# Kernel optimization log

Hardware: AMD Instinct MI355X
Metric: run time of the kernel (lower is better)

## Reference

```python
import jax, jax.numpy as jnp
import numpy as np

N_NODES = 20000
N_INPUT = 64
K_MAX = 12
BITS = 64
N_OUT = 10
BATCH = 64
T = 128


def setup_inputs() -> dict:
    key = jax.random.key(0)
    ks = jax.random.split(key, 8)
    x = jax.random.randint(ks[0], (BATCH, T, BITS), 0, 2, dtype=jnp.int32)
    w_in = jax.random.randint(ks[1], (BITS, N_INPUT), 0, 2, dtype=jnp.int32)
    adj_list = jax.random.randint(ks[2], (N_NODES, K_MAX), 0, N_NODES, dtype=jnp.int32)
    adj_mask = jax.random.randint(ks[3], (N_NODES, K_MAX), 0, 2, dtype=jnp.int32)
    lut = jax.random.randint(ks[4], (N_NODES, 2 ** K_MAX), 0, 2, dtype=jnp.int32)
    init_states = jax.random.randint(ks[5], (1, N_NODES), 0, 2, dtype=jnp.int32)
    W_out = jax.random.normal(ks[6], (N_OUT, N_NODES - N_INPUT), dtype=jnp.float32) * 0.02
    b_out = jnp.zeros((N_OUT,), dtype=jnp.float32)
    return {"x": x, "w_in": w_in, "adj_list": adj_list, "adj_mask": adj_mask,
            "lut": lut, "init_states": init_states, "W_out": W_out, "b_out": b_out}


def reference(x, w_in, adj_list, adj_mask, lut, init_states, W_out, b_out):
    B, T_, bits = x.shape
    N, k = adj_list.shape
    I = w_in.shape[1]
    # powers_of_2, big-endian order as in make_minimal_powers_of_two (flip)
    powers = (2 ** jnp.arange(k - 1, -1, -1)).astype(jnp.int32)  # [k]
    no_neigh = ~(adj_mask.astype(bool).any(axis=1))              # [N] nodes w/o neighbours keep state
    node_ids = jnp.arange(N)
    states0 = jnp.broadcast_to(init_states, (B, N)).astype(jnp.int32)

    def step(states, x_t):
        # inject input: bipartite mapping of input bits onto first I nodes (OR-combine)
        u = ((x_t @ w_in) > 0).astype(jnp.int32)                 # [B, I]
        states = states.at[:, :I].set(u)
        # gather incoming neighbour states per node (irregular gather)
        neigh = jnp.take(states, adj_list, axis=1)               # [B, N, k]
        neigh = neigh * adj_mask[None, :, :]
        # bit-pack into LUT index
        idx = (neigh * powers[None, None, :]).sum(axis=-1)       # [B, N], < 2^k
        new = lut[node_ids[None, :], idx]                        # [B, N] LUT lookup
        new = jnp.where(no_neigh[None, :], states, new)
        return new, None

    states, _ = jax.lax.scan(step, states0, jnp.swapaxes(x, 0, 1))
    # readout on reservoir (non-input) nodes at final timestep
    feats = states[:, I:].astype(jnp.float32)                    # [B, N-I]
    out = jax.nn.sigmoid(feats @ W_out.T + b_out)                # [B, n_outputs]
    return out
```

## Files before the change

### kernel.cpp

```cpp
#include <hip/hip_runtime.h>
#include <cstdint>
#include <cstddef>


#define N_NODES   20000
#define N_INPUT   64
#define K_MAX     12
#define T_STEPS   128
#define N_BATCH   64
#define N_OUT     10
#define N_FEAT    (N_NODES - N_INPUT)
#define DUMMY_NODE 20000
#define ST_WORDS  20004

#define NBLK 256
#define NTHR 1024
#define NPB  78
#define NPB_PAD 80
#define LEAF_CNT 64
#define GO_CNT  8
#define BAR_STRIDE 32
#define ROOT_IDX 64

typedef unsigned long long u64;

__global__ __launch_bounds__(256) void pack_x_kernel(const int* __restrict__ x,
                                                     u64* __restrict__ xp) {
  const int t = blockIdx.x;
  const int wave = threadIdx.x >> 6, lane = threadIdx.x & 63;
  for (int b = wave; b < N_BATCH; b += 4) {
    int v = x[((size_t)b * T_STEPS + t) * 64 + lane];
    u64 bal = __ballot(v != 0);
    if (lane == 0) xp[(size_t)t * N_BATCH + b] = bal;
  }
}

__global__ __launch_bounds__(256) void init_kernel(const int* __restrict__ inis,
                                                   const int* __restrict__ w_in,
                                                   u64* __restrict__ buf0,
                                                   u64* __restrict__ buf1,
                                                   u64* __restrict__ wcol,
                                                   unsigned* __restrict__ bar) {
  if (blockIdx.x < 79) {
    int n = blockIdx.x * 256 + threadIdx.x;
    if (n >= N_INPUT && n < ST_WORDS) {
      u64 w = (n < N_NODES && inis[n] != 0) ? ~0ull : 0ull;
      buf0[n] = w;
      buf1[n] = w;
    }
  } else {
    const int wave = threadIdx.x >> 6, lane = threadIdx.x & 63;
    for (int i = wave; i < 64; i += 4) {
      int wv = w_in[(size_t)lane * 64 + i];
      u64 wc = __ballot(wv != 0);
      if (lane == 0) wcol[i] = wc;
    }
    if (threadIdx.x < ROOT_IDX + 1 + GO_CNT)
      bar[threadIdx.x * BAR_STRIDE] = 0u;
  }
}

__global__ __launch_bounds__(64) void u_pre_kernel(const u64* __restrict__ xp,
                                                   const u64* __restrict__ wcol,
                                                   u64* __restrict__ u_all) {
  const int t = blockIdx.x, lane = threadIdx.x;
  u64 xw = xp[(size_t)t * N_BATCH + lane];
  for (int i = 0; i < 64; i++) {
    u64 ub = __ballot((xw & wcol[i]) != 0);
    if (lane == 0) u_all[(size_t)t * 64 + i] = ub;
  }
}

__device__ __forceinline__ u64 bit_transpose64(u64 w, int lane) {
  const u64 LO0 = 0x00000000FFFFFFFFull, LO1 = 0x0000FFFF0000FFFFull,
            LO2 = 0x00FF00FF00FF00FFull, LO3 = 0x0F0F0F0F0F0F0F0Full,
            LO4 = 0x3333333333333333ull, LO5 = 0x5555555555555555ull;
#define XP_STAGE(d, LO)                                                  \
  {                                                                      \
    u64 p = (u64)__shfl_xor((long long)w, (d), 64);                      \
    if (lane & (d)) w = ((p >> (d)) & (LO)) | (w & ~(LO));               \
    else            w = (w & (LO)) | ((p << (d)) & ~(LO));               \
  }
  XP_STAGE(32, LO0) XP_STAGE(16, LO1) XP_STAGE(8, LO2)
  XP_STAGE(4,  LO3) XP_STAGE(2,  LO4) XP_STAGE(1, LO5)
#undef XP_STAGE
  return w;
}

__global__ __launch_bounds__(NTHR) void reservoir_kernel(
    const int* __restrict__ lut, const int* __restrict__ adj,
    const int* __restrict__ mask, const u64* __restrict__ u_all,
    u64* __restrict__ buf0, u64* __restrict__ buf1,
    unsigned* __restrict__ bar) {
  __shared__ u64 lut_lds[NPB_PAD * 64];
  __shared__ int adj_lds[NPB_PAD * K_MAX];
  __shared__ unsigned char hn_lds[NPB_PAD];

  const int bi = blockIdx.x;
  const int tid = threadIdx.x;
  const int wave = tid >> 6, lane = tid & 63;
  const int base = N_INPUT + bi * NPB;
  const int nloc = min(NPB, N_NODES - base);

  if (tid < NPB_PAD) {
    int i = tid, h = 0;
    if (i < nloc) {
      for (int j = 0; j < K_MAX; j++) {
        int m = mask[(size_t)(base + i) * K_MAX + j];
        int a = adj[(size_t)(base + i) * K_MAX + j];
        adj_lds[i * K_MAX + (K_MAX - 1 - j)] = m ? a : DUMMY_NODE;
        h |= m;
      }
    } else {
      for (int j = 0; j < K_MAX; j++) adj_lds[i * K_MAX + j] = DUMMY_NODE;
    }
    hn_lds[i] = (unsigned char)(h ? 1 : 0);
  }

  const int nwords = nloc * 64;
  const int* lp = lut + (size_t)base * 4096;
  for (int w0 = wave * 8; w0 < nwords; w0 += 128) {
    int v[8];
#pragma unroll
    for (int q = 0; q < 8; q++) {
      int widx = w0 + q;
      v[q] = (widx < nwords) ? lp[(size_t)widx * 64 + lane] : 0;
    }
#pragma unroll
    for (int q = 0; q < 8; q++) {
      int widx = w0 + q;
      u64 bal = __ballot(v[q] != 0);
      if (lane == 0 && widx < nwords) lut_lds[widx] = bal;
    }
  }
  __syncthreads();

  const int l0 = wave * 5;
  const int cnt = min(5, nloc - l0);
  const bool do_store = (lane < cnt) && hn_lds[l0 + lane];

  for (int t = 0; t < T_STEPS; t++) {
    u64* cur = (t & 1) ? buf1 : buf0;
    u64* nxt = (t & 1) ? buf0 : buf1;
    const u64* ubase = u_all + (size_t)t * 64;

    u64 w = 0;
    if (lane < 60) {
      int a = adj_lds[l0 * K_MAX + lane];
      const u64* p = (a < N_INPUT) ? (ubase + a) : (cur + a);
      w = __hip_atomic_load(p, __ATOMIC_RELAXED, __HIP_MEMORY_SCOPE_AGENT);
    }
    w = bit_transpose64(w, lane);

    u64 keep = 0;
#pragma unroll
    for (int i = 0; i < 5; i++) {
      if (i < cnt) {
        unsigned idx = (unsigned)(w >> (12 * i)) & 0xFFFu;
        u64 g = lut_lds[(l0 + i) * 64 + (idx >> 6)];
        u64 res = __ballot((g >> (idx & 63)) & 1ull);
        if (lane == i) keep = res;
      }
    }
    if (do_store)
      __hip_atomic_store(&nxt[base + l0 + lane], keep,
                         __ATOMIC_RELAXED, __HIP_MEMORY_SCOPE_AGENT);

    if (t != T_STEPS - 1) {
      __syncthreads();
      __builtin_amdgcn_fence(__ATOMIC_RELEASE, "workgroup");
      if (wave == 0) {
        unsigned leafold = 0;
        if (lane == 0)
          leafold = __hip_atomic_fetch_add(&bar[(bi & (LEAF_CNT - 1)) * BAR_STRIDE],
                                           1u, __ATOMIC_RELAXED, __HIP_MEMORY_SCOPE_AGENT);
        leafold = (unsigned)__shfl((int)leafold, 0);
        if (leafold == (unsigned)t * (NBLK / LEAF_CNT) + (NBLK / LEAF_CNT - 1)) {
          unsigned rootold = 0;
          if (lane == 0)
            rootold = __hip_atomic_fetch_add(&bar[ROOT_IDX * BAR_STRIDE], 1u,
                                             __ATOMIC_RELAXED, __HIP_MEMORY_SCOPE_AGENT);
          rootold = (unsigned)__shfl((int)rootold, 0);
          if (rootold == (unsigned)t * LEAF_CNT + (LEAF_CNT - 1) && lane < GO_CNT)
            __hip_atomic_store(&bar[(ROOT_IDX + 1 + lane) * BAR_STRIDE],
                               (unsigned)(t + 1),
                               __ATOMIC_RELAXED, __HIP_MEMORY_SCOPE_AGENT);
        }
        unsigned* gp = &bar[(ROOT_IDX + 1 + (bi & (GO_CNT - 1))) * BAR_STRIDE];
        while (__hip_atomic_load(gp, __ATOMIC_RELAXED, __HIP_MEMORY_SCOPE_AGENT)
               < (unsigned)(t + 1))
          __builtin_amdgcn_s_sleep(1);
      }
      __builtin_amdgcn_fence(__ATOMIC_ACQUIRE, "workgroup");
      __syncthreads();
    }
  }
}

__global__ __launch_bounds__(256) void readout_kernel(const u64* __restrict__ st,
                                                      const float* __restrict__ Wout,
                                                      const float* __restrict__ bout,
                                                      float* __restrict__ out) {
  const int b = blockIdx.x / N_OUT;
  const int o = blockIdx.x % N_OUT;
  float acc = 0.f;
  for (int n = threadIdx.x; n < N_FEAT; n += 256) {
    u64 s = st[N_INPUT + n];
    float w = Wout[(size_t)o * N_FEAT + n];
    acc += ((s >> b) & 1ull) ? w : 0.f;
  }
  for (int off = 32; off > 0; off >>= 1) acc += __shfl_down(acc, off);
  __shared__ float red[4];
  const int wave = threadIdx.x >> 6, lane = threadIdx.x & 63;
  if (lane == 0) red[wave] = acc;
  __syncthreads();
  if (threadIdx.x == 0) {
    float tot = red[0] + red[1] + red[2] + red[3] + bout[o];
    out[(size_t)b * N_OUT + o] = 1.f / (1.f + __expf(-tot));
  }
}

extern "C" void kernel_launch(void* const* d_in, const int* in_sizes, int n_in,
                              void* d_out, int out_size, void* d_ws, size_t ws_size,
                              hipStream_t stream) {
  const int* x    = (const int*)d_in[0];
  const int* w_in = (const int*)d_in[1];
  const int* adj  = (const int*)d_in[2];
  const int* mask = (const int*)d_in[3];
  const int* lut  = (const int*)d_in[4];
  const int* inis = (const int*)d_in[5];
  const float* Wout = (const float*)d_in[6];
  const float* bout = (const float*)d_in[7];
  float* out = (float*)d_out;

  char* ws = (char*)d_ws;
  size_t off = 0;
  auto alloc = [&](size_t bytes) -> void* {
    void* p = ws + off;
    off += (bytes + 255) & ~(size_t)255;
    return p;
  };
  u64* buf0 = (u64*)alloc((size_t)ST_WORDS * 8);
  u64* buf1 = (u64*)alloc((size_t)ST_WORDS * 8);
  u64* xp   = (u64*)alloc((size_t)T_STEPS * N_BATCH * 8);
  u64* wcol = (u64*)alloc(64 * 8);
  u64* u_all = (u64*)alloc((size_t)T_STEPS * 64 * 8);
  unsigned* bar = (unsigned*)alloc((size_t)(ROOT_IDX + 1 + GO_CNT) * BAR_STRIDE * 4);
  (void)ws_size; (void)in_sizes; (void)n_in; (void)out_size;

  hipLaunchKernelGGL(pack_x_kernel, dim3(T_STEPS), dim3(256), 0, stream, x, xp);
  hipLaunchKernelGGL(init_kernel, dim3(80), dim3(256), 0, stream,
                     inis, w_in, buf0, buf1, wcol, bar);
  hipLaunchKernelGGL(u_pre_kernel, dim3(T_STEPS), dim3(64), 0, stream,
                     xp, wcol, u_all);

  void* args[] = {(void*)&lut, (void*)&adj, (void*)&mask, (void*)&u_all,
                  (void*)&buf0, (void*)&buf1, (void*)&bar};
  hipLaunchCooperativeKernel((const void*)reservoir_kernel,
                             dim3(NBLK), dim3(NTHR), args, 0, stream);

  hipLaunchKernelGGL(readout_kernel, dim3(N_BATCH * N_OUT), dim3(256), 0, stream,
                     buf0, Wout, bout, out);
}
```

Baseline: 1.061 ms.

## Replace per-step grid barrier with tagged ring-buffer dataflow sync

Each node state is split into two 64-bit words that carry 32 state bits and the timestep as a tag. Consumers spin on their neighbour loads until the tags match, which replaces the per-step global tree barrier. An 8-deep ring of state buffers lets blocks run ahead, so a flat arrival/go barrier is needed only every 6 steps to keep writers from overwriting slots still being read. This trades barrier latency for twice the gather loads, possible repeated polling of stale words, and a bounded spin guard that could silently return stale data.

```diff
diff --git a/kernel.cpp b/kernel.cpp
--- a/kernel.cpp
+++ b/kernel.cpp
@@ -17,12 +17,15 @@
 #define NTHR 1024
 #define NPB  78
 #define NPB_PAD 80
-#define LEAF_CNT 64
-#define GO_CNT  8
-#define BAR_STRIDE 32
-#define ROOT_IDX 64
+#define R_BUF 8
+#define M_BAR 6
+#define GO_CNT 8
+#define AS     32
 
 typedef unsigned long long u64;
+
+#define A_LOAD(p)    __hip_atomic_load((p), __ATOMIC_RELAXED, __HIP_MEMORY_SCOPE_AGENT)
+#define A_STORE(p,v) __hip_atomic_store((p), (v), __ATOMIC_RELAXED, __HIP_MEMORY_SCOPE_AGENT)
 
 __global__ __launch_bounds__(256) void pack_x_kernel(const int* __restrict__ x,
                                                      u64* __restrict__ xp) {
@@ -37,26 +40,34 @@
 
 __global__ __launch_bounds__(256) void init_kernel(const int* __restrict__ inis,
                                                    const int* __restrict__ w_in,
-                                                   u64* __restrict__ buf0,
-                                                   u64* __restrict__ buf1,
+                                                   const u64* __restrict__ xp,
+                                                   u64* __restrict__ Ar,
+                                                   u64* __restrict__ Br,
                                                    u64* __restrict__ wcol,
-                                                   unsigned* __restrict__ bar) {
+                                                   unsigned* __restrict__ arr,
+                                                   unsigned* __restrict__ go) {
   if (blockIdx.x < 79) {
     int n = blockIdx.x * 256 + threadIdx.x;
     if (n >= N_INPUT && n < ST_WORDS) {
       u64 w = (n < N_NODES && inis[n] != 0) ? ~0ull : 0ull;
-      buf0[n] = w;
-      buf1[n] = w;
+      Ar[n] = (w & 0xFFFFFFFFull) << 32;
+      Br[n] = (w >> 32) << 32;
     }
   } else {
     const int wave = threadIdx.x >> 6, lane = threadIdx.x & 63;
+    u64 xw = xp[lane];
     for (int i = wave; i < 64; i += 4) {
       int wv = w_in[(size_t)lane * 64 + i];
       u64 wc = __ballot(wv != 0);
       if (lane == 0) wcol[i] = wc;
-    }
-    if (threadIdx.x < ROOT_IDX + 1 + GO_CNT)
-      bar[threadIdx.x * BAR_STRIDE] = 0u;
+      u64 ub = __ballot((xw & wc) != 0);
+      if (lane == 0) {
+        Ar[i] = (ub & 0xFFFFFFFFull) << 32;
+        Br[i] = (ub >> 32) << 32;
+      }
+    }
+    arr[threadIdx.x * AS] = 0u;
+    if (threadIdx.x < GO_CNT) go[threadIdx.x * AS] = 0u;
   }
 }
 
@@ -89,12 +100,14 @@
 
 __global__ __launch_bounds__(NTHR) void reservoir_kernel(
     const int* __restrict__ lut, const int* __restrict__ adj,
-    const int* __restrict__ mask, const u64* __restrict__ u_all,
-    u64* __restrict__ buf0, u64* __restrict__ buf1,
-    unsigned* __restrict__ bar) {
+    const int* __restrict__ mask, const int* __restrict__ inis,
+    const u64* __restrict__ u_all, u64* __restrict__ Aring,
+    u64* __restrict__ Bring, unsigned* __restrict__ arr,
+    unsigned* __restrict__ go) {
   __shared__ u64 lut_lds[NPB_PAD * 64];
   __shared__ int adj_lds[NPB_PAD * K_MAX];
   __shared__ unsigned char hn_lds[NPB_PAD];
+  __shared__ volatile unsigned lds_scan[4];
 
   const int bi = blockIdx.x;
   const int tid = threadIdx.x;
@@ -116,6 +129,7 @@
     }
     hn_lds[i] = (unsigned char)(h ? 1 : 0);
   }
+  if (tid < 4) lds_scan[tid] = 0u;
 
   const int nwords = nloc * 64;
   const int* lp = lut + (size_t)base * 4096;
@@ -136,68 +150,104 @@
   __syncthreads();
 
   const int l0 = wave * 5;
-  const int cnt = min(5, nloc - l0);
-  const bool do_store = (lane < cnt) && hn_lds[l0 + lane];
-
-  for (int t = 0; t < T_STEPS; t++) {
-    u64* cur = (t & 1) ? buf1 : buf0;
-    u64* nxt = (t & 1) ? buf0 : buf1;
-    const u64* ubase = u_all + (size_t)t * 64;
-
-    u64 w = 0;
-    if (lane < 60) {
-      int a = adj_lds[l0 * K_MAX + lane];
-      const u64* p = (a < N_INPUT) ? (ubase + a) : (cur + a);
-      w = __hip_atomic_load(p, __ATOMIC_RELAXED, __HIP_MEMORY_SCOPE_AGENT);
-    }
-    w = bit_transpose64(w, lane);
-
-    u64 keep = 0;
+  const int cnt5 = min(5, nloc - l0);
+  const int a_reg = (lane < 60) ? adj_lds[l0 * K_MAX + lane] : DUMMY_NODE;
+  u64 mystate = 0;
+  if (cnt5 > 0 && lane < cnt5)
+    mystate = (inis[base + l0 + lane] != 0) ? ~0ull : 0ull;
+
+  for (int s = 0; s < T_STEPS; s++) {
+    const unsigned tg = (unsigned)s;
+    const u64* Ac = Aring + (size_t)(s & 7) * ST_WORDS;
+    const u64* Bc = Bring + (size_t)(s & 7) * ST_WORDS;
+    u64 newS = 0;
+
+    if (cnt5 > 0) {
+      u64 va = 0, vb = 0;
+      if (lane < 60) {
+        va = A_LOAD(Ac + a_reg);
+        vb = A_LOAD(Bc + a_reg);
+      }
+      int guard = 0;
+      for (;;) {
+        bool stale = (lane < 60) &&
+                     (((unsigned)va != tg) || ((unsigned)vb != tg));
+        if (!__any(stale)) break;
+        if (++guard > (1 << 17)) break;
+        if (stale) {
+          va = A_LOAD(Ac + a_reg);
+          vb = A_LOAD(Bc + a_reg);
+        }
+      }
+      u64 w64 = (va >> 32) | (vb & 0xFFFFFFFF00000000ull);
+      w64 = bit_transpose64(w64, lane);
+
+      u64 keep = 0;
 #pragma unroll
-    for (int i = 0; i < 5; i++) {
-      if (i < cnt) {
-        unsigned idx = (unsigned)(w >> (12 * i)) & 0xFFFu;
-        u64 g = lut_lds[(l0 + i) * 64 + (idx >> 6)];
-        u64 res = __ballot((g >> (idx & 63)) & 1ull);
-        if (lane == i) keep = res;
-      }
-    }
-    if (do_store)
-      __hip_atomic_store(&nxt[base + l0 + lane], keep,
-                         __ATOMIC_RELAXED, __HIP_MEMORY_SCOPE_AGENT);
-
-    if (t != T_STEPS - 1) {
+      for (int i = 0; i < 5; i++) {
+        if (i < cnt5) {
+          unsigned idx = (unsigned)(w64 >> (12 * i)) & 0xFFFu;
+          u64 g = lut_lds[(l0 + i) * 64 + (idx >> 6)];
+          u64 res = __ballot((g >> (idx & 63)) & 1ull);
+          if (lane == i) keep = res;
+        }
+      }
+      if (lane < cnt5) {
+        newS = hn_lds[l0 + lane] ? keep : mystate;
+        mystate = newS;
+      }
+    }
+
+    const unsigned tg1 = (unsigned)(s + 1);
+    u64* An = Aring + (size_t)((s + 1) & 7) * ST_WORDS;
+    u64* Bn = Bring + (size_t)((s + 1) & 7) * ST_WORDS;
+    if (cnt5 > 0) {
+      u64 Sv = (u64)__shfl((long long)newS, lane & 7);
+      bool stl = ((lane & 7) < cnt5) && (lane < 16) && ((lane & 7) == lane || lane >= 8);
+      u64 word = (lane < 8) ? (((Sv & 0xFFFFFFFFull) << 32) | tg1)
+                            : (((Sv >> 32) << 32) | tg1);
+      u64* p = ((lane < 8) ? An : Bn) + (base + l0 + (lane & 7));
+      if (stl) A_STORE(p, word);
+    } else if (bi == NBLK - 1 && wave == 10) {
+      if (s + 1 < T_STEPS) {
+        u64 S = u_all[(size_t)(s + 1) * 64 + lane];
+        A_STORE(&An[lane], ((S & 0xFFFFFFFFull) << 32) | tg1);
+        A_STORE(&Bn[lane], ((S >> 32) << 32) | tg1);
+      }
+    } else if (bi == NBLK - 1 && wave == 11) {
+      if (lane == 0 && s + 1 < T_STEPS) {
+        A_STORE(&An[DUMMY_NODE], (u64)tg1);
+        A_STORE(&Bn[DUMMY_NODE], (u64)tg1);
+      }
+    }
+
+    if (s != T_STEPS - 1 && (s % M_BAR) == (M_BAR - 1)) {
+      const unsigned e = (unsigned)(s / M_BAR) + 1;
       __syncthreads();
-      __builtin_amdgcn_fence(__ATOMIC_RELEASE, "workgroup");
+      if (wave == 0 && lane == 0) A_STORE(&arr[bi * AS], e);
+      if (bi == 0 && wave < 4) {
+        const int idx = (wave * 64 + lane) * AS;
+        for (;;) {
+          unsigned v = A_LOAD(&arr[idx]);
+          if (__all(v >= e)) break;
+        }
+        if (lane == 0) lds_scan[wave] = e;
+      }
+      if (bi == 0 && wave == 0) {
+        while (lds_scan[0] < e || lds_scan[1] < e ||
+               lds_scan[2] < e || lds_scan[3] < e) {}
+        if (lane < GO_CNT) A_STORE(&go[lane * AS], e);
+      }
       if (wave == 0) {
-        unsigned leafold = 0;
-        if (lane == 0)
-          leafold = __hip_atomic_fetch_add(&bar[(bi & (LEAF_CNT - 1)) * BAR_STRIDE],
-                                           1u, __ATOMIC_RELAXED, __HIP_MEMORY_SCOPE_AGENT);
-        leafold = (unsigned)__shfl((int)leafold, 0);
-        if (leafold == (unsigned)t * (NBLK / LEAF_CNT) + (NBLK / LEAF_CNT - 1)) {
-          unsigned rootold = 0;
-          if (lane == 0)
-            rootold = __hip_atomic_fetch_add(&bar[ROOT_IDX * BAR_STRIDE], 1u,
-                                             __ATOMIC_RELAXED, __HIP_MEMORY_SCOPE_AGENT);
-          rootold = (unsigned)__shfl((int)rootold, 0);
-          if (rootold == (unsigned)t * LEAF_CNT + (LEAF_CNT - 1) && lane < GO_CNT)
-            __hip_atomic_store(&bar[(ROOT_IDX + 1 + lane) * BAR_STRIDE],
-                               (unsigned)(t + 1),
-                               __ATOMIC_RELAXED, __HIP_MEMORY_SCOPE_AGENT);
-        }
-        unsigned* gp = &bar[(ROOT_IDX + 1 + (bi & (GO_CNT - 1))) * BAR_STRIDE];
-        while (__hip_atomic_load(gp, __ATOMIC_RELAXED, __HIP_MEMORY_SCOPE_AGENT)
-               < (unsigned)(t + 1))
-          __builtin_amdgcn_s_sleep(1);
-      }
-      __builtin_amdgcn_fence(__ATOMIC_ACQUIRE, "workgroup");
+        while (A_LOAD(&go[(bi & (GO_CNT - 1)) * AS]) < e) {}
+      }
       __syncthreads();
     }
   }
 }
 
-__global__ __launch_bounds__(256) void readout_kernel(const u64* __restrict__ st,
+__global__ __launch_bounds__(256) void readout_kernel(const u64* __restrict__ Ar,
+                                                      const u64* __restrict__ Br,
                                                       const float* __restrict__ Wout,
                                                       const float* __restrict__ bout,
                                                       float* __restrict__ out) {
@@ -205,7 +255,7 @@
   const int o = blockIdx.x % N_OUT;
   float acc = 0.f;
   for (int n = threadIdx.x; n < N_FEAT; n += 256) {
-    u64 s = st[N_INPUT + n];
+    u64 s = (Ar[N_INPUT + n] >> 32) | ((Br[N_INPUT + n] >> 32) << 32);
     float w = Wout[(size_t)o * N_FEAT + n];
     acc += ((s >> b) & 1ull) ? w : 0.f;
   }
@@ -240,25 +290,27 @@
     off += (bytes + 255) & ~(size_t)255;
     return p;
   };
-  u64* buf0 = (u64*)alloc((size_t)ST_WORDS * 8);
-  u64* buf1 = (u64*)alloc((size_t)ST_WORDS * 8);
-  u64* xp   = (u64*)alloc((size_t)T_STEPS * N_BATCH * 8);
-  u64* wcol = (u64*)alloc(64 * 8);
+  u64* Aring = (u64*)alloc((size_t)R_BUF * ST_WORDS * 8);
+  u64* Bring = (u64*)alloc((size_t)R_BUF * ST_WORDS * 8);
+  u64* xp    = (u64*)alloc((size_t)T_STEPS * N_BATCH * 8);
+  u64* wcol  = (u64*)alloc(64 * 8);
   u64* u_all = (u64*)alloc((size_t)T_STEPS * 64 * 8);
-  unsigned* bar = (unsigned*)alloc((size_t)(ROOT_IDX + 1 + GO_CNT) * BAR_STRIDE * 4);
+  unsigned* arr = (unsigned*)alloc((size_t)NBLK * AS * 4);
+  unsigned* go  = (unsigned*)alloc((size_t)GO_CNT * AS * 4);
   (void)ws_size; (void)in_sizes; (void)n_in; (void)out_size;
 
   hipLaunchKernelGGL(pack_x_kernel, dim3(T_STEPS), dim3(256), 0, stream, x, xp);
   hipLaunchKernelGGL(init_kernel, dim3(80), dim3(256), 0, stream,
-                     inis, w_in, buf0, buf1, wcol, bar);
+                     inis, w_in, xp, Aring, Bring, wcol, arr, go);
   hipLaunchKernelGGL(u_pre_kernel, dim3(T_STEPS), dim3(64), 0, stream,
                      xp, wcol, u_all);
 
-  void* args[] = {(void*)&lut, (void*)&adj, (void*)&mask, (void*)&u_all,
-                  (void*)&buf0, (void*)&buf1, (void*)&bar};
+  void* args[] = {(void*)&lut, (void*)&adj, (void*)&mask, (void*)&inis,
+                  (void*)&u_all, (void*)&Aring, (void*)&Bring,
+                  (void*)&arr, (void*)&go};
   hipLaunchCooperativeKernel((const void*)reservoir_kernel,
                              dim3(NBLK), dim3(NTHR), args, 0, stream);
 
   hipLaunchKernelGGL(readout_kernel, dim3(N_BATCH * N_OUT), dim3(256), 0, stream,
-                     buf0, Wout, bout, out);
-}
+                     Aring, Bring, Wout, bout, out);
+}
```

New measurement: 1.569 ms. +47.8%, slower.
